# Performance work log

Measured on AMD Instinct MI355X. Metric: run time of the kernel, lower is better.

The kernel has to match this reference:

```python
import jax, jax.numpy as jnp
import numpy as np


def _rope(v, pos, head_dim):
    # v: [H, D]; rotate consecutive pairs by angle pos * theta_j
    theta = 1.0 / (10000.0 ** (jnp.arange(0, head_dim, 2, dtype=jnp.float32) / head_dim))
    ang = pos * theta                      # [D/2]
    cos, sin = jnp.cos(ang), jnp.sin(ang)
    vr = v.reshape(v.shape[0], -1, 2)      # [H, D/2, 2]
    re = vr[..., 0] * cos - vr[..., 1] * sin
    im = vr[..., 0] * sin + vr[..., 1] * cos
    return jnp.stack([re, im], axis=-1).reshape(v.shape)


def setup_inputs() -> dict:
    key = jax.random.key(0)
    ks = jax.random.split(key, 7)
    dim, H, D, S = 4096, 32, 128, 2048
    scale = 0.02
    return {
        "x": jax.random.normal(ks[0], (dim,), dtype=jnp.float32),
        "wq": jax.random.normal(ks[1], (dim, dim), dtype=jnp.float32) * scale,
        "wk": jax.random.normal(ks[2], (dim, dim), dtype=jnp.float32) * scale,
        "wv": jax.random.normal(ks[3], (dim, dim), dtype=jnp.float32) * scale,
        "wo": jax.random.normal(ks[4], (dim, dim), dtype=jnp.float32) * scale,
        "cache_k": jax.random.normal(ks[5], (S, H, D), dtype=jnp.float32),
        "cache_v": jax.random.normal(ks[6], (S, H, D), dtype=jnp.float32),
        "pos": 1536,
    }


def reference(x, wq, wk, wv, wo, cache_k, cache_v, pos):
    H, D = cache_k.shape[1], cache_k.shape[2]
    # nn.Linear without bias: y = W @ x
    xq = (wq @ x).reshape(H, D)
    xk = (wk @ x).reshape(H, D)
    xv = (wv @ x).reshape(H, D)
    xq = _rope(xq, pos, D)
    xk = _rope(xk, pos, D)
    # KV cache append (pos is a static Python int)
    cache_k = cache_k.at[pos].set(xk)
    cache_v = cache_v.at[pos].set(xv)
    keys = cache_k[: pos + 1]              # [P, H, D]
    values = cache_v[: pos + 1]            # [P, H, D]
    # single-query decode attention per head
    scores = jnp.einsum("hd,phd->hp", xq, keys) / jnp.sqrt(jnp.float32(D))
    scores = jax.nn.softmax(scores, axis=-1)
    out = jnp.einsum("hp,phd->hd", scores, values)   # [H, D]
    return wo @ out.reshape(-1)
```

## Files before the change

### kernel.cpp

```cpp
#include <hip/hip_runtime.h>
#include <math.h>

#define DIM 4096
#define H 32
#define D 128
#define SMAX 2048
#define CHUNK 32
#define NCHUNK (SMAX / CHUNK)
#define PART_STRIDE 132

typedef float v4f __attribute__((ext_vector_type(4)));

__device__ __forceinline__ float wave_sum(float v) {
#pragma unroll
    for (int o = 32; o; o >>= 1) v += __shfl_xor(v, o);
    return v;
}

__global__ void __launch_bounds__(256) qkv_rope(
        const float* __restrict__ wq, const float* __restrict__ wk,
        const float* __restrict__ wv, const float* __restrict__ x,
        const int* __restrict__ pos_p,
        float* __restrict__ xq, float* __restrict__ xk, float* __restrict__ xv) {
    __shared__ float red[2][4];
    int t = threadIdx.x, lane = t & 63, w = t >> 6;
    int b = blockIdx.x;
    int mat = b >> 11;
    int pr  = b & 2047;
    const float* wm = (mat == 0) ? wq : ((mat == 1) ? wk : wv);
    const float* base = wm + (size_t)pr * 2 * DIM;

    float a0 = 0.f, a1 = 0.f, a2 = 0.f, a3 = 0.f;
    float b0 = 0.f, b1 = 0.f, b2 = 0.f, b3 = 0.f;
#pragma unroll
    for (int i = 0; i < 4; ++i) {
        int idx = i * 1024 + t * 4;
        v4f wa = *reinterpret_cast<const v4f*>(base + idx);
        v4f wb = *reinterpret_cast<const v4f*>(base + DIM + idx);
        v4f xr = *reinterpret_cast<const v4f*>(x + idx);
        a0 = fmaf(wa.x, xr.x, a0);
        a1 = fmaf(wa.y, xr.y, a1);
        a2 = fmaf(wa.z, xr.z, a2);
        a3 = fmaf(wa.w, xr.w, a3);
        b0 = fmaf(wb.x, xr.x, b0);
        b1 = fmaf(wb.y, xr.y, b1);
        b2 = fmaf(wb.z, xr.z, b2);
        b3 = fmaf(wb.w, xr.w, b3);
    }
    float da = wave_sum((a0 + a1) + (a2 + a3));
    float db = wave_sum((b0 + b1) + (b2 + b3));
    if (lane == 0) { red[0][w] = da; red[1][w] = db; }
    __syncthreads();
    if (t == 0) {
        float d0 = red[0][0] + red[0][1] + red[0][2] + red[0][3];
        float d1 = red[1][0] + red[1][1] + red[1][2] + red[1][3];
        if (mat == 2) {
            xv[2 * pr] = d0; xv[2 * pr + 1] = d1;
        } else {
            int pos = *pos_p;
            int j = pr & 63;
            float theta = powf(10000.0f, -(float)(2 * j) / (float)D);
            float ang = (float)pos * theta;
            float s, c;
            sincosf(ang, &s, &c);
            float* o = (mat == 0) ? xq : xk;
            o[2 * pr]     = d0 * c - d1 * s;
            o[2 * pr + 1] = d0 * s + d1 * c;
        }
    }
}

__global__ void attn_partial(const float* __restrict__ cache_k, const float* __restrict__ cache_v,
                             const float* __restrict__ xq, const float* __restrict__ xk,
                             const float* __restrict__ xv, const int* __restrict__ pos_p,
                             float* __restrict__ partials) {
    __shared__ float lds_m[4], lds_l[4];
    __shared__ float lds_acc[4][128];
    int h = blockIdx.x;
    int c = blockIdx.y;
    int lane = threadIdx.x;
    int g  = lane >> 4;
    int gl = lane & 15;
    int pos = *pos_p;
    int base = c * CHUNK;
    int p1 = min(base + CHUNK, pos + 1);
    float* pp = partials + (size_t)(h * NCHUNK + c) * PART_STRIDE;

    if (base > pos) {
        if (lane == 0) { pp[128] = -INFINITY; pp[129] = 0.f; }
        reinterpret_cast<float2*>(pp)[lane] = make_float2(0.f, 0.f);
        return;
    }

    const float4* qv = reinterpret_cast<const float4*>(xq + h * D + gl * 8);
    const float4 q0 = qv[0], q1 = qv[1];

    float m = -INFINITY, l = 0.f;
    float4 acc0 = make_float4(0.f, 0.f, 0.f, 0.f);
    float4 acc1 = make_float4(0.f, 0.f, 0.f, 0.f);

    for (int p = base + g; p < p1; p += 4) {
        const float* kp = (p == pos) ? (xk + h * D)
                                     : (cache_k + ((size_t)p * H + h) * D);
        const float4* kv4 = reinterpret_cast<const float4*>(kp + gl * 8);
        float4 k0 = kv4[0], k1 = kv4[1];
        float d = q0.x * k0.x + q0.y * k0.y + q0.z * k0.z + q0.w * k0.w
                + q1.x * k1.x + q1.y * k1.y + q1.z * k1.z + q1.w * k1.w;
        d += __shfl_xor(d, 1);
        d += __shfl_xor(d, 2);
        d += __shfl_xor(d, 4);
        d += __shfl_xor(d, 8);
        float s = d * 0.08838834764831845f;
        float mn = fmaxf(m, s);
        float corr = __expf(m - mn);
        float wgt  = __expf(s - mn);
        const float* vp = (p == pos) ? (xv + h * D)
                                     : (cache_v + ((size_t)p * H + h) * D);
        const float4* vv4 = reinterpret_cast<const float4*>(vp + gl * 8);
        float4 v0 = vv4[0], v1 = vv4[1];
        l = l * corr + wgt;
        acc0.x = fmaf(wgt, v0.x, acc0.x * corr);
        acc0.y = fmaf(wgt, v0.y, acc0.y * corr);
        acc0.z = fmaf(wgt, v0.z, acc0.z * corr);
        acc0.w = fmaf(wgt, v0.w, acc0.w * corr);
        acc1.x = fmaf(wgt, v1.x, acc1.x * corr);
        acc1.y = fmaf(wgt, v1.y, acc1.y * corr);
        acc1.z = fmaf(wgt, v1.z, acc1.z * corr);
        acc1.w = fmaf(wgt, v1.w, acc1.w * corr);
        m = mn;
    }

    if (gl == 0) { lds_m[g] = m; lds_l[g] = l; }
    *reinterpret_cast<float4*>(&lds_acc[g][gl * 8])     = acc0;
    *reinterpret_cast<float4*>(&lds_acc[g][gl * 8 + 4]) = acc1;
    __syncthreads();
    float M = fmaxf(fmaxf(lds_m[0], lds_m[1]), fmaxf(lds_m[2], lds_m[3]));
    float w0 = __expf(lds_m[0] - M);
    float w1 = __expf(lds_m[1] - M);
    float w2 = __expf(lds_m[2] - M);
    float w3 = __expf(lds_m[3] - M);
    float L  = w0 * lds_l[0] + w1 * lds_l[1] + w2 * lds_l[2] + w3 * lds_l[3];
    int d0 = 2 * lane;
    float s0 = w0 * lds_acc[0][d0]     + w1 * lds_acc[1][d0]
             + w2 * lds_acc[2][d0]     + w3 * lds_acc[3][d0];
    float s1 = w0 * lds_acc[0][d0 + 1] + w1 * lds_acc[1][d0 + 1]
             + w2 * lds_acc[2][d0 + 1] + w3 * lds_acc[3][d0 + 1];
    if (lane == 0) { pp[128] = M; pp[129] = L; }
    reinterpret_cast<float2*>(pp)[lane] = make_float2(s0, s1);
}

__global__ void attn_combine(const float* __restrict__ partials, float* __restrict__ out_attn) {
    int h = blockIdx.x;
    int lane = threadIdx.x;
    float m = -INFINITY;
    for (int c = 0; c < NCHUNK; ++c)
        m = fmaxf(m, partials[(size_t)(h * NCHUNK + c) * PART_STRIDE + 128]);
    float L = 0.f, a0 = 0.f, a1 = 0.f;
    for (int c = 0; c < NCHUNK; ++c) {
        const float* pp = partials + (size_t)(h * NCHUNK + c) * PART_STRIDE;
        float mw = pp[128];
        float w = (mw == -INFINITY) ? 0.f : __expf(mw - m);
        L += pp[129] * w;
        float2 a = *reinterpret_cast<const float2*>(pp + 2 * lane);
        a0 += w * a.x;
        a1 += w * a.y;
    }
    float inv = 1.f / L;
    out_attn[h * D + 2 * lane]     = a0 * inv;
    out_attn[h * D + 2 * lane + 1] = a1 * inv;
}

__device__ __forceinline__ void load_half(v4f (&buf)[8], const float* __restrict__ wp, int off) {
#pragma unroll
    for (int i = 0; i < 8; ++i)
        buf[i] = *reinterpret_cast<const v4f*>(wp + i * 256 + off);
}

template <int XO>
__device__ __forceinline__ float dot_half(const v4f (&buf)[8], const v4f (&xr)[16]) {
    float s0 = 0.f, s1 = 0.f, s2 = 0.f, s3 = 0.f;
#pragma unroll
    for (int i = 0; i < 8; ++i) {
        s0 = fmaf(buf[i].x, xr[XO + i].x, s0);
        s1 = fmaf(buf[i].y, xr[XO + i].y, s1);
        s2 = fmaf(buf[i].z, xr[XO + i].z, s2);
        s3 = fmaf(buf[i].w, xr[XO + i].w, s3);
    }
    return (s0 + s1) + (s2 + s3);
}

#define SB() __builtin_amdgcn_sched_barrier(0)

__global__ void __launch_bounds__(256) matvec_o(
        const float* __restrict__ w_, const float* __restrict__ vin,
        float* __restrict__ y) {
    int t = threadIdx.x, lane = t & 63;
    int W = blockIdx.x * 4 + (t >> 6);
    int r0 = W * 2;
    int off = lane * 4;

    v4f xr[16];
#pragma unroll
    for (int i = 0; i < 16; ++i)
        xr[i] = *reinterpret_cast<const v4f*>(vin + i * 256 + off);

    const float* w0 = w_ + (size_t)r0 * DIM;
    v4f A[8], B[8];
    float d0, d1;
    load_half(A, w0, off);
    load_half(B, w0 + 2048, off);            SB();
    d0  = dot_half<0>(A, xr);
    load_half(A, w0 + DIM, off);             SB();
    d0 += dot_half<8>(B, xr);
    load_half(B, w0 + DIM + 2048, off);      SB();
    d1  = dot_half<0>(A, xr);
    d1 += dot_half<8>(B, xr);

    d0 = wave_sum(d0); d1 = wave_sum(d1);
    if (lane == 0) { y[r0] = d0; y[r0 + 1] = d1; }
}

extern "C" void kernel_launch(void* const* d_in, const int* in_sizes, int n_in,
                              void* d_out, int out_size, void* d_ws, size_t ws_size,
                              hipStream_t stream) {
    const float* x       = (const float*)d_in[0];
    const float* wq      = (const float*)d_in[1];
    const float* wk      = (const float*)d_in[2];
    const float* wv      = (const float*)d_in[3];
    const float* wo      = (const float*)d_in[4];
    const float* cache_k = (const float*)d_in[5];
    const float* cache_v = (const float*)d_in[6];
    const int*   pos     = (const int*)d_in[7];

    float* wsf      = (float*)d_ws;
    float* xq       = wsf;
    float* xk       = wsf + DIM;
    float* xv       = wsf + 2 * DIM;
    float* partials = wsf + 3 * DIM;
    float* out_attn = partials + H * NCHUNK * PART_STRIDE;
    float* y        = (float*)d_out;

    qkv_rope<<<3 * 2048, 256, 0, stream>>>(wq, wk, wv, x, pos, xq, xk, xv);
    attn_partial<<<dim3(H, NCHUNK), 64, 0, stream>>>(cache_k, cache_v, xq, xk, xv, pos, partials);
    attn_combine<<<H, 64, 0, stream>>>(partials, out_attn);
    matvec_o<<<512, 256, 0, stream>>>(wo, out_attn, y);
}
```

Baseline: 80.59 us.

## Assign one row pair per wavefront and stage x in shared memory

```diff
diff --git a/kernel.cpp b/kernel.cpp
--- a/kernel.cpp
+++ b/kernel.cpp
@@ -17,27 +17,34 @@
     return v;
 }
 
-__global__ void __launch_bounds__(256) qkv_rope(
+__global__ void __launch_bounds__(256) qkv_stream(
         const float* __restrict__ wq, const float* __restrict__ wk,
         const float* __restrict__ wv, const float* __restrict__ x,
         const int* __restrict__ pos_p,
         float* __restrict__ xq, float* __restrict__ xk, float* __restrict__ xv) {
-    __shared__ float red[2][4];
+    __shared__ float xs[DIM];
     int t = threadIdx.x, lane = t & 63, w = t >> 6;
-    int b = blockIdx.x;
-    int mat = b >> 11;
-    int pr  = b & 2047;
+
+#pragma unroll
+    for (int i = 0; i < 4; ++i)
+        *reinterpret_cast<v4f*>(&xs[(i * 256 + t) * 4]) =
+            *reinterpret_cast<const v4f*>(x + (i * 256 + t) * 4);
+    __syncthreads();
+
+    int task = blockIdx.x * 4 + w;
+    int mat = task >> 11;
+    int pr  = task & 2047;
     const float* wm = (mat == 0) ? wq : ((mat == 1) ? wk : wv);
     const float* base = wm + (size_t)pr * 2 * DIM;
 
     float a0 = 0.f, a1 = 0.f, a2 = 0.f, a3 = 0.f;
     float b0 = 0.f, b1 = 0.f, b2 = 0.f, b3 = 0.f;
 #pragma unroll
-    for (int i = 0; i < 4; ++i) {
-        int idx = i * 1024 + t * 4;
+    for (int k = 0; k < 16; ++k) {
+        int idx = (k * 64 + lane) * 4;
         v4f wa = *reinterpret_cast<const v4f*>(base + idx);
         v4f wb = *reinterpret_cast<const v4f*>(base + DIM + idx);
-        v4f xr = *reinterpret_cast<const v4f*>(x + idx);
+        v4f xr = *reinterpret_cast<const v4f*>(&xs[idx]);
         a0 = fmaf(wa.x, xr.x, a0);
         a1 = fmaf(wa.y, xr.y, a1);
         a2 = fmaf(wa.z, xr.z, a2);
@@ -49,13 +56,10 @@
     }
     float da = wave_sum((a0 + a1) + (a2 + a3));
     float db = wave_sum((b0 + b1) + (b2 + b3));
-    if (lane == 0) { red[0][w] = da; red[1][w] = db; }
-    __syncthreads();
-    if (t == 0) {
-        float d0 = red[0][0] + red[0][1] + red[0][2] + red[0][3];
-        float d1 = red[1][0] + red[1][1] + red[1][2] + red[1][3];
+
+    if (lane == 0) {
         if (mat == 2) {
-            xv[2 * pr] = d0; xv[2 * pr + 1] = d1;
+            xv[2 * pr] = da; xv[2 * pr + 1] = db;
         } else {
             int pos = *pos_p;
             int j = pr & 63;
@@ -64,8 +68,8 @@
             float s, c;
             sincosf(ang, &s, &c);
             float* o = (mat == 0) ? xq : xk;
-            o[2 * pr]     = d0 * c - d1 * s;
-            o[2 * pr + 1] = d0 * s + d1 * c;
+            o[2 * pr]     = da * c - db * s;
+            o[2 * pr + 1] = da * s + db * c;
         }
     }
 }
@@ -240,7 +244,7 @@
     float* out_attn = partials + H * NCHUNK * PART_STRIDE;
     float* y        = (float*)d_out;
 
-    qkv_rope<<<3 * 2048, 256, 0, stream>>>(wq, wk, wv, x, pos, xq, xk, xv);
+    qkv_stream<<<1536, 256, 0, stream>>>(wq, wk, wv, x, pos, xq, xk, xv);
     attn_partial<<<dim3(H, NCHUNK), 64, 0, stream>>>(cache_k, cache_v, xq, xk, xv, pos, partials);
     attn_combine<<<H, 64, 0, stream>>>(partials, out_attn);
     matvec_o<<<512, 256, 0, stream>>>(wo, out_attn, y);
```

Result: faster. 77.18 us (-4.2%).
